# Optimization experiments

Hardware: AMD Instinct MI355X
Metric: run time of the kernel (lower is better)

## Reference

```python
import jax, jax.numpy as jnp
import numpy as np


def _mlp(h, weights, biases, n_relu):
    # Linear(+ReLU) stack; ReLU on the first n_relu layers, final layer linear only.
    for i, (w, b) in enumerate(zip(weights, biases)):
        h = h @ w + b
        if i < n_relu:
            h = jax.nn.relu(h)
    return h


def setup_inputs() -> dict:
    key = jax.random.key(0)
    ks = jax.random.split(key, 12)
    B, M, E = 16384, 512, 1024

    def lin(k, fan_in, fan_out):
        # xavier-ish scaling so activations stay well-conditioned
        return jax.random.normal(k, (fan_in, fan_out), jnp.float32) * (1.0 / np.sqrt(fan_in))

    return {
        "x": jax.random.normal(ks[0], (B, M), jnp.float32),
        "rand_noise": jax.random.uniform(ks[1], (B, M), jnp.float32),
        "u_random": jax.random.uniform(ks[2], (B, M), jnp.float32),
        "marginals_min": jnp.zeros((M,), jnp.float32),
        "marginals_max": jnp.ones((M,), jnp.float32),
        "enc_w0": lin(ks[3], M, E), "enc_b0": jnp.full((E,), 0.01, jnp.float32),
        "enc_w1": lin(ks[4], E, E), "enc_b1": jnp.full((E,), 0.01, jnp.float32),
        "enc_w2": lin(ks[5], E, E), "enc_b2": jnp.full((E,), 0.01, jnp.float32),
        "enc_w3": lin(ks[6], E, E), "enc_b3": jnp.full((E,), 0.01, jnp.float32),
        "head_w0": lin(ks[7], E, E), "head_b0": jnp.full((E,), 0.01, jnp.float32),
        "head_w1": lin(ks[8], E, E), "head_b1": jnp.full((E,), 0.01, jnp.float32),
        "corruption_len": 307,
    }


def reference(x, rand_noise, u_random, marginals_min, marginals_max,
              enc_w0, enc_b0, enc_w1, enc_b1, enc_w2, enc_b2, enc_w3, enc_b3,
              head_w0, head_b0, head_w1, head_b1, corruption_len):
    B, M = x.shape
    # Vectorized equivalent of per-row randperm(m)[:corruption_len]:
    # top-k of iid uniform noise picks a uniform random subset of size k per row.
    _, idx = jax.lax.top_k(rand_noise, corruption_len)            # [B, k]
    mask = jnp.zeros((B, M), bool).at[jnp.arange(B)[:, None], idx].set(True)

    # Marginal samples ~ Uniform(min, max) per feature.
    x_random = marginals_min + u_random * (marginals_max - marginals_min)
    x_corrupted = jnp.where(mask, x_random, x)

    enc_ws = [enc_w0, enc_w1, enc_w2, enc_w3]
    enc_bs = [enc_b0, enc_b1, enc_b2, enc_b3]
    head_ws = [head_w0, head_w1]
    head_bs = [head_b0, head_b1]

    # Run both branches through one batched pass (same math, fewer launches).
    both = jnp.concatenate([x, x_corrupted], axis=0)              # [2B, M]
    h = _mlp(both, enc_ws, enc_bs, n_relu=3)                      # encoder depth 4
    h = _mlp(h, head_ws, head_bs, n_relu=1)                       # head depth 2
    embeddings, embeddings_corrupted = h[:B], h[B:]
    return embeddings, embeddings_corrupted
```

## Files before the change

### kernel.cpp

```cpp
#include <hip/hip_runtime.h>

typedef _Float16 f16x8 __attribute__((ext_vector_type(8)));
typedef float f32x4 __attribute__((ext_vector_type(4)));

__device__ __forceinline__ void gload16(const void* g, void* l) {
  __builtin_amdgcn_global_load_lds(
      (const __attribute__((address_space(1))) void*)g,
      (__attribute__((address_space(3))) void*)l, 16, 0, 0);
}

__device__ __forceinline__ void barfence() {
  asm volatile("" ::: "memory");
  __builtin_amdgcn_s_barrier();
  asm volatile("" ::: "memory");
}

__device__ __forceinline__ int xcd_swz(int orig, int nwg) {
  int q = nwg >> 3, r = nwg & 7;
  int x = orig & 7, loc = orig >> 3;
  int base = (x < r) ? x * (q + 1) : r * (q + 1) + (x - r) * q;
  return base + loc;
}

struct WPtrs { const float* w[6]; _Float16* wt[6]; };
__global__ __launch_bounds__(256) void transpose_all(WPtrs p) {
  const int N = 1024;
  __shared__ float tile[32][33];
  int y = blockIdx.y, layer, ky;
  if (y < 16) { layer = 0; ky = y; }
  else { int t = y - 16; layer = 1 + (t >> 5); ky = t & 31; }
  int K = (layer == 0) ? 512 : 1024;
  const float* W = p.w[layer];
  _Float16* WT = p.wt[layer];
  int tx = threadIdx.x, ty = threadIdx.y;
  int n0 = blockIdx.x * 32, k0 = ky * 32;
#pragma unroll
  for (int i = 0; i < 4; i++)
    tile[ty + i * 8][tx] = W[(long)(k0 + ty + i * 8) * N + (n0 + tx)];
  __syncthreads();
#pragma unroll
  for (int i = 0; i < 4; i++)
    WT[(long)(n0 + ty + i * 8) * K + (k0 + tx)] = (_Float16)tile[tx][ty + i * 8];
}

__global__ __launch_bounds__(256) void cast_f16(const float* __restrict__ in,
                                                _Float16* __restrict__ out, long n) {
  long i = ((long)blockIdx.x * 256 + threadIdx.x) * 4;
  if (i < n) {
    float4 v = *(const float4*)(in + i);
    typedef _Float16 f16x4 __attribute__((ext_vector_type(4)));
    f16x4 o = {(_Float16)v.x, (_Float16)v.y, (_Float16)v.z, (_Float16)v.w};
    *(f16x4*)(out + i) = o;
  }
}

__global__ __launch_bounds__(256) void topk_corrupt(
    const float* __restrict__ noise, const float* __restrict__ x,
    const float* __restrict__ u, const float* __restrict__ mmin,
    const float* __restrict__ mmax, const int* __restrict__ kptr,
    _Float16* __restrict__ dplain, _Float16* __restrict__ dcorr,
    int xrow0, int nrows) {
  int lane = threadIdx.x & 63;
  int r = (blockIdx.x << 2) + (threadIdx.x >> 6);
  if (r >= nrows) return;
  long row = (long)xrow0 + r;
  long rb = row * 512 + lane * 8;
  float4 n0 = *(const float4*)(noise + rb);
  float4 n1 = *(const float4*)(noise + rb + 4);
  unsigned v[8] = {__float_as_uint(n0.x), __float_as_uint(n0.y),
                   __float_as_uint(n0.z), __float_as_uint(n0.w),
                   __float_as_uint(n1.x), __float_as_uint(n1.y),
                   __float_as_uint(n1.z), __float_as_uint(n1.w)};
  int kk = *kptr;
  unsigned T = 0;
  for (int bit = 30; bit >= 0; --bit) {
    unsigned Tp = T | (1u << bit);
    int c = 0;
#pragma unroll
    for (int j = 0; j < 8; j++) c += (int)__popcll(__ballot(v[j] >= Tp));
    if (c >= kk) T = Tp;
  }
  int cgt = 0;
  unsigned long long eqb[8];
#pragma unroll
  for (int j = 0; j < 8; j++) {
    cgt += (int)__popcll(__ballot(v[j] > T));
    eqb[j] = __ballot(v[j] == T);
  }
  int need = kk - cgt;
  unsigned long long below = (1ull << lane) - 1ull;
  int rank_base = 0;
#pragma unroll
  for (int j = 0; j < 8; j++) rank_base += (int)__popcll(eqb[j] & below);

  float4 x0 = *(const float4*)(x + rb);
  float4 x1 = *(const float4*)(x + rb + 4);
  float4 u0 = *(const float4*)(u + rb);
  float4 u1 = *(const float4*)(u + rb + 4);
  int col = lane * 8;
  float4 mn0 = *(const float4*)(mmin + col);
  float4 mn1 = *(const float4*)(mmin + col + 4);
  float4 mx0 = *(const float4*)(mmax + col);
  float4 mx1 = *(const float4*)(mmax + col + 4);
  float xs[8] = {x0.x, x0.y, x0.z, x0.w, x1.x, x1.y, x1.z, x1.w};
  float us[8] = {u0.x, u0.y, u0.z, u0.w, u1.x, u1.y, u1.z, u1.w};
  float mns[8] = {mn0.x, mn0.y, mn0.z, mn0.w, mn1.x, mn1.y, mn1.z, mn1.w};
  float mxs[8] = {mx0.x, mx0.y, mx0.z, mx0.w, mx1.x, mx1.y, mx1.z, mx1.w};

  f16x8 po, co;
  int loc = 0;
#pragma unroll
  for (int j = 0; j < 8; j++) {
    bool eq = (v[j] == T);
    int rank = rank_base + loc;
    bool m = (v[j] > T) || (eq && (rank < need));
    loc += eq ? 1 : 0;
    float rv = mns[j] + us[j] * (mxs[j] - mns[j]);
    float cv = m ? rv : xs[j];
    po[j] = (_Float16)xs[j];
    co[j] = (_Float16)cv;
  }
  long ob = (long)r * 512 + lane * 8;
  if (dplain) *(f16x8*)(dplain + ob) = po;
  *(f16x8*)(dcorr + ob) = co;
}

template <bool RELU, bool OUTF32>
__global__ __launch_bounds__(512, 2) void gemm8p(const _Float16* __restrict__ A,
                                                 const _Float16* __restrict__ BT,
                                                 const float* __restrict__ bias,
                                                 void* __restrict__ Cout, int K) {
  const int N = 1024;
  __shared__ _Float16 S[2][4][8192];
  int tid = threadIdx.x;
  int lane = tid & 63, wave = tid >> 6;
  int wr = wave >> 2, wc = wave & 3;
  int logical = xcd_swz(blockIdx.x, gridDim.x);
  long arow0 = (long)(logical >> 2) * 256;
  int bcol0 = (logical & 3) * 256;

  int srow = tid >> 3;
  int scg = (tid & 7) ^ (srow & 7);
  const _Float16* gA[2][2];
  const _Float16* gB[2][2];
#pragma unroll
  for (int h = 0; h < 2; h++)
#pragma unroll
    for (int j = 0; j < 2; j++) {
      gA[h][j] = A + (arow0 + h * 128 + j * 64 + srow) * (long)K + scg * 8;
      gB[h][j] = BT + (long)(bcol0 + h * 128 + j * 64 + srow) * K + scg * 8;
    }
  int lo = tid * 8;

#define STG_A(BUF, H, T)                                   \
  do {                                                     \
    gload16(gA[H][0] + (T) * 64, &S[BUF][H][lo]);          \
    gload16(gA[H][1] + (T) * 64, &S[BUF][H][4096 + lo]);   \
  } while (0)
#define STG_B(BUF, H, T)                                      \
  do {                                                        \
    gload16(gB[H][0] + (T) * 64, &S[BUF][2 + H][lo]);         \
    gload16(gB[H][1] + (T) * 64, &S[BUF][2 + H][4096 + lo]);  \
  } while (0)

  int lr = lane & 15, g = lane >> 4, e = lr & 7;
  int cs0 = ((0 * 4 + g) ^ e) * 8;
  int cs1 = ((1 * 4 + g) ^ e) * 8;
  int aoff[4], boff[2];
#pragma unroll
  for (int mf = 0; mf < 4; mf++) aoff[mf] = (wr * 64 + mf * 16 + lr) * 64;
#pragma unroll
  for (int nf = 0; nf < 2; nf++) boff[nf] = (wc * 32 + nf * 16 + lr) * 64;

  f16x8 af0[4][2], af1[4][2];
  f16x8 bf0[2][2], bf1[2][2];
  f32x4 acc[2][2][4][2] = {};

#define LDA(DST, BUF, MQ)                                            \
  do {                                                               \
    _Pragma("unroll") for (int mf = 0; mf < 4; mf++) {               \
      DST[mf][0] = *(const f16x8*)&S[BUF][MQ][aoff[mf] + cs0];       \
      DST[mf][1] = *(const f16x8*)&S[BUF][MQ][aoff[mf] + cs1];       \
    }                                                                \
  } while (0)
#define LDB(DST, BUF, NQ)                                            \
  do {                                                               \
    _Pragma("unroll") for (int nf = 0; nf < 2; nf++) {               \
      DST[nf][0] = *(const f16x8*)&S[BUF][2 + NQ][boff[nf] + cs0];   \
      DST[nf][1] = *(const f16x8*)&S[BUF][2 + NQ][boff[nf] + cs1];   \
    }                                                                \
  } while (0)
#define MFMA_Q(AF, BF, MQ, NQ)                                       \
  do {                                                               \
    __builtin_amdgcn_s_setprio(1);                                   \
    _Pragma("unroll") for (int mf = 0; mf < 4; mf++)                 \
    _Pragma("unroll") for (int nf = 0; nf < 2; nf++)                 \
    _Pragma("unroll") for (int kk = 0; kk < 2; kk++)                 \
      acc[MQ][NQ][mf][nf] = __builtin_amdgcn_mfma_f32_16x16x32_f16(  \
          AF[mf][kk], BF[nf][kk], acc[MQ][NQ][mf][nf], 0, 0, 0);     \
    __builtin_amdgcn_s_setprio(0);                                   \
  } while (0)

  int NT = K / 64;
  STG_B(0, 0, 0); STG_B(0, 1, 0); STG_A(0, 0, 0); STG_A(0, 1, 0);
  asm volatile("s_waitcnt vmcnt(2)" ::: "memory");
  barfence();
  LDA(af0, 0, 0);
  LDB(bf1, 0, 1);

  for (int t = 0; t < NT; ++t) {
    int buf = t & 1, nbuf = buf ^ 1;
    LDB(bf0, buf, 0);
    if (t + 1 < NT) { STG_B(nbuf, 0, t + 1); STG_B(nbuf, 1, t + 1); }
    MFMA_Q(af0, bf0, 0, 0);
    if (t + 1 < NT) asm volatile("s_waitcnt vmcnt(4)" ::: "memory");
    else            asm volatile("s_waitcnt vmcnt(0)" ::: "memory");
    barfence();
    LDA(af1, buf, 1);
    if (t + 1 < NT) STG_A(nbuf, 0, t + 1);
    MFMA_Q(af0, bf1, 0, 1);
    barfence();
    if (t + 1 < NT) STG_A(nbuf, 1, t + 1);
    MFMA_Q(af1, bf1, 1, 1);
    if (t + 1 < NT) asm volatile("s_waitcnt vmcnt(2)" ::: "memory");
    barfence();
    if (t + 1 < NT) { LDA(af0, nbuf, 0); LDB(bf1, nbuf, 1); }
    MFMA_Q(af1, bf0, 1, 0);
    if (t + 1 < NT) barfence();
  }
#undef STG_A
#undef STG_B
#undef LDA
#undef LDB
#undef MFMA_Q

  int r0 = (lane >> 4) * 4;
  float bv[2][2];
#pragma unroll
  for (int nq = 0; nq < 2; nq++)
#pragma unroll
    for (int nf = 0; nf < 2; nf++)
      bv[nq][nf] = bias[bcol0 + nq * 128 + wc * 32 + nf * 16 + lr];
#pragma unroll
  for (int mq = 0; mq < 2; mq++)
#pragma unroll
    for (int mf = 0; mf < 4; mf++) {
      long rowb = arow0 + mq * 128 + wr * 64 + mf * 16 + r0;
#pragma unroll
      for (int nq = 0; nq < 2; nq++)
#pragma unroll
        for (int nf = 0; nf < 2; nf++) {
          int col = bcol0 + nq * 128 + wc * 32 + nf * 16 + lr;
#pragma unroll
          for (int rr = 0; rr < 4; rr++) {
            float v = acc[mq][nq][mf][nf][rr] + bv[nq][nf];
            if (RELU) v = fmaxf(v, 0.f);
            if (OUTF32) ((float*)Cout)[(rowb + rr) * N + col] = v;
            else ((_Float16*)Cout)[(rowb + rr) * N + col] = (_Float16)v;
          }
        }
    }
}

extern "C" void kernel_launch(void* const* d_in, const int* in_sizes, int n_in,
                              void* d_out, int out_size, void* d_ws, size_t ws_size,
                              hipStream_t stream) {
  const float* x    = (const float*)d_in[0];
  const float* rn   = (const float*)d_in[1];
  const float* ur   = (const float*)d_in[2];
  const float* mmin = (const float*)d_in[3];
  const float* mmax = (const float*)d_in[4];
  const float* W[6]  = {(const float*)d_in[5],  (const float*)d_in[7],  (const float*)d_in[9],
                        (const float*)d_in[11], (const float*)d_in[13], (const float*)d_in[15]};
  const float* Bi[6] = {(const float*)d_in[6],  (const float*)d_in[8],  (const float*)d_in[10],
                        (const float*)d_in[12], (const float*)d_in[14], (const float*)d_in[16]};
  const int* kptr = (const int*)d_in[17];
  float* out = (float*)d_out;

  const long B = 16384;
  const int E = 1024;
  const int Ks[6] = {512, 1024, 1024, 1024, 1024, 1024};

  char* ws = (char*)d_ws;
  _Float16* wT[6];
  size_t off = 0;
  for (int i = 0; i < 6; i++) { wT[i] = (_Float16*)(ws + off); off += (size_t)Ks[i] * E * 2; }
  size_t rem = (ws_size > off) ? ws_size - off : 0;
  long R = 32768;
  while (R > 256 && (size_t)R * 5120 > rem) R >>= 1;

  _Float16* bothc = (_Float16*)(ws + off);
  _Float16* h0 = bothc + R * 512;
  _Float16* h1 = h0 + R * 1024;

  WPtrs wp;
  for (int i = 0; i < 6; i++) { wp.w[i] = W[i]; wp.wt[i] = wT[i]; }
  transpose_all<<<dim3(E / 32, 16 + 5 * 32), dim3(32, 8), 0, stream>>>(wp);

  for (long r0 = 0; r0 < 2 * B; r0 += R) {
    if (R == 2 * B) {
      topk_corrupt<<<dim3((unsigned)(B / 4)), dim3(256), 0, stream>>>(
          rn, x, ur, mmin, mmax, kptr, bothc, bothc + B * 512, 0, (int)B);
    } else {
      long plainEnd = (r0 < B) ? ((r0 + R < B) ? (r0 + R) : B) : r0;
      long p1 = plainEnd - r0;
      if (p1 > 0) {
        long n = p1 * 512;
        long blocks = (n / 4 + 255) / 256;
        cast_f16<<<dim3((unsigned)blocks), dim3(256), 0, stream>>>(x + r0 * 512, bothc, n);
      }
      long c0 = (r0 > B) ? r0 : B;
      long p2 = (r0 + R) - c0;
      if (p2 > 0) {
        topk_corrupt<<<dim3((unsigned)((p2 + 3) / 4)), dim3(256), 0, stream>>>(
            rn, x, ur, mmin, mmax, kptr, (_Float16*)nullptr,
            bothc + (c0 - r0) * 512, (int)(c0 - B), (int)p2);
      }
    }
    dim3 gg((unsigned)((R / 256) * 4)), gb(512);
    gemm8p<true,  false><<<gg, gb, 0, stream>>>(bothc, wT[0], Bi[0], (void*)h0, 512);
    gemm8p<true,  false><<<gg, gb, 0, stream>>>(h0,    wT[1], Bi[1], (void*)h1, 1024);
    gemm8p<true,  false><<<gg, gb, 0, stream>>>(h1,    wT[2], Bi[2], (void*)h0, 1024);
    gemm8p<false, false><<<gg, gb, 0, stream>>>(h0,    wT[3], Bi[3], (void*)h1, 1024);
    gemm8p<true,  false><<<gg, gb, 0, stream>>>(h1,    wT[4], Bi[4], (void*)h0, 1024);
    gemm8p<false, true ><<<gg, gb, 0, stream>>>(h0,    wT[5], Bi[5],
                                                 (void*)(out + r0 * 1024), 1024);
  }
}
```

Before: 404.7 us.

## Shrink GEMM tiles to 128x128, fuse transpose with top-k prep, nontemporal output

Cuts the GEMM block tile from 256x256 to 128x128 with half the LDS and a launch bound allowing 4 blocks per CU. This raises the block count and occupancy at the cost of less data reuse per block. The weight transpose and the top-k/corruption prep are merged into one launch, and the final fp32 output is written with nontemporal stores. The waitcnt values are retuned for fewer loads per stage.

```diff
diff --git a/kernel.cpp b/kernel.cpp
--- a/kernel.cpp
+++ b/kernel.cpp
@@ -23,47 +23,13 @@
 }
 
 struct WPtrs { const float* w[6]; _Float16* wt[6]; };
-__global__ __launch_bounds__(256) void transpose_all(WPtrs p) {
-  const int N = 1024;
-  __shared__ float tile[32][33];
-  int y = blockIdx.y, layer, ky;
-  if (y < 16) { layer = 0; ky = y; }
-  else { int t = y - 16; layer = 1 + (t >> 5); ky = t & 31; }
-  int K = (layer == 0) ? 512 : 1024;
-  const float* W = p.w[layer];
-  _Float16* WT = p.wt[layer];
-  int tx = threadIdx.x, ty = threadIdx.y;
-  int n0 = blockIdx.x * 32, k0 = ky * 32;
-#pragma unroll
-  for (int i = 0; i < 4; i++)
-    tile[ty + i * 8][tx] = W[(long)(k0 + ty + i * 8) * N + (n0 + tx)];
-  __syncthreads();
-#pragma unroll
-  for (int i = 0; i < 4; i++)
-    WT[(long)(n0 + ty + i * 8) * K + (k0 + tx)] = (_Float16)tile[tx][ty + i * 8];
-}
-
-__global__ __launch_bounds__(256) void cast_f16(const float* __restrict__ in,
-                                                _Float16* __restrict__ out, long n) {
-  long i = ((long)blockIdx.x * 256 + threadIdx.x) * 4;
-  if (i < n) {
-    float4 v = *(const float4*)(in + i);
-    typedef _Float16 f16x4 __attribute__((ext_vector_type(4)));
-    f16x4 o = {(_Float16)v.x, (_Float16)v.y, (_Float16)v.z, (_Float16)v.w};
-    *(f16x4*)(out + i) = o;
-  }
-}
-
-__global__ __launch_bounds__(256) void topk_corrupt(
+
+__device__ __forceinline__ void topk_row(
     const float* __restrict__ noise, const float* __restrict__ x,
     const float* __restrict__ u, const float* __restrict__ mmin,
-    const float* __restrict__ mmax, const int* __restrict__ kptr,
-    _Float16* __restrict__ dplain, _Float16* __restrict__ dcorr,
-    int xrow0, int nrows) {
+    const float* __restrict__ mmax, int kk, _Float16* __restrict__ dplain,
+    _Float16* __restrict__ dcorr, long row, long orow) {
   int lane = threadIdx.x & 63;
-  int r = (blockIdx.x << 2) + (threadIdx.x >> 6);
-  if (r >= nrows) return;
-  long row = (long)xrow0 + r;
   long rb = row * 512 + lane * 8;
   float4 n0 = *(const float4*)(noise + rb);
   float4 n1 = *(const float4*)(noise + rb + 4);
@@ -71,7 +37,6 @@
                    __float_as_uint(n0.z), __float_as_uint(n0.w),
                    __float_as_uint(n1.x), __float_as_uint(n1.y),
                    __float_as_uint(n1.z), __float_as_uint(n1.w)};
-  int kk = *kptr;
   unsigned T = 0;
   for (int bit = 30; bit >= 0; --bit) {
     unsigned Tp = T | (1u << bit);
@@ -120,90 +85,151 @@
     po[j] = (_Float16)xs[j];
     co[j] = (_Float16)cv;
   }
-  long ob = (long)r * 512 + lane * 8;
+  long ob = orow * 512 + lane * 8;
   if (dplain) *(f16x8*)(dplain + ob) = po;
   *(f16x8*)(dcorr + ob) = co;
 }
 
+__global__ __launch_bounds__(256) void prep_all(
+    const float* __restrict__ noise, const float* __restrict__ x,
+    const float* __restrict__ u, const float* __restrict__ mmin,
+    const float* __restrict__ mmax, const int* __restrict__ kptr,
+    _Float16* __restrict__ dplain, _Float16* __restrict__ dcorr,
+    WPtrs p, int ntopk) {
+  const int N = 1024;
+  if ((int)blockIdx.x < ntopk) {
+    int r = ((int)blockIdx.x << 2) + (threadIdx.x >> 6);
+    topk_row(noise, x, u, mmin, mmax, *kptr, dplain, dcorr, r, r);
+    return;
+  }
+  int b = (int)blockIdx.x - ntopk;
+  int bx = b & 31;
+  int y = b >> 5;
+  __shared__ float tile[32][33];
+  int layer, ky;
+  if (y < 16) { layer = 0; ky = y; }
+  else { int t = y - 16; layer = 1 + (t >> 5); ky = t & 31; }
+  int K = (layer == 0) ? 512 : 1024;
+  const float* W = p.w[layer];
+  _Float16* WT = p.wt[layer];
+  int tx = threadIdx.x & 31, ty = threadIdx.x >> 5;
+  int n0 = bx * 32, k0 = ky * 32;
+#pragma unroll
+  for (int i = 0; i < 4; i++)
+    tile[ty + i * 8][tx] = W[(long)(k0 + ty + i * 8) * N + (n0 + tx)];
+  __syncthreads();
+#pragma unroll
+  for (int i = 0; i < 4; i++)
+    WT[(long)(n0 + ty + i * 8) * K + (k0 + tx)] = (_Float16)tile[tx][ty + i * 8];
+}
+
+__global__ __launch_bounds__(256) void transpose_all(WPtrs p) {
+  const int N = 1024;
+  __shared__ float tile[32][33];
+  int y = blockIdx.y, layer, ky;
+  if (y < 16) { layer = 0; ky = y; }
+  else { int t = y - 16; layer = 1 + (t >> 5); ky = t & 31; }
+  int K = (layer == 0) ? 512 : 1024;
+  const float* W = p.w[layer];
+  _Float16* WT = p.wt[layer];
+  int tx = threadIdx.x, ty = threadIdx.y;
+  int n0 = blockIdx.x * 32, k0 = ky * 32;
+#pragma unroll
+  for (int i = 0; i < 4; i++)
+    tile[ty + i * 8][tx] = W[(long)(k0 + ty + i * 8) * N + (n0 + tx)];
+  __syncthreads();
+#pragma unroll
+  for (int i = 0; i < 4; i++)
+    WT[(long)(n0 + ty + i * 8) * K + (k0 + tx)] = (_Float16)tile[tx][ty + i * 8];
+}
+
+__global__ __launch_bounds__(256) void cast_f16(const float* __restrict__ in,
+                                                _Float16* __restrict__ out, long n) {
+  long i = ((long)blockIdx.x * 256 + threadIdx.x) * 4;
+  if (i < n) {
+    float4 v = *(const float4*)(in + i);
+    typedef _Float16 f16x4 __attribute__((ext_vector_type(4)));
+    f16x4 o = {(_Float16)v.x, (_Float16)v.y, (_Float16)v.z, (_Float16)v.w};
+    *(f16x4*)(out + i) = o;
+  }
+}
+
+__global__ __launch_bounds__(256) void topk_corrupt(
+    const float* __restrict__ noise, const float* __restrict__ x,
+    const float* __restrict__ u, const float* __restrict__ mmin,
+    const float* __restrict__ mmax, const int* __restrict__ kptr,
+    _Float16* __restrict__ dcorr, int xrow0, int nrows) {
+  int r = ((int)blockIdx.x << 2) + (threadIdx.x >> 6);
+  if (r >= nrows) return;
+  topk_row(noise, x, u, mmin, mmax, *kptr, (_Float16*)nullptr, dcorr,
+           (long)xrow0 + r, r);
+}
+
 template <bool RELU, bool OUTF32>
-__global__ __launch_bounds__(512, 2) void gemm8p(const _Float16* __restrict__ A,
+__global__ __launch_bounds__(512, 4) void gemmtp(const _Float16* __restrict__ A,
                                                  const _Float16* __restrict__ BT,
                                                  const float* __restrict__ bias,
                                                  void* __restrict__ Cout, int K) {
   const int N = 1024;
-  __shared__ _Float16 S[2][4][8192];
+  __shared__ _Float16 S[2][4][4096];
   int tid = threadIdx.x;
   int lane = tid & 63, wave = tid >> 6;
   int wr = wave >> 2, wc = wave & 3;
   int logical = xcd_swz(blockIdx.x, gridDim.x);
-  long arow0 = (long)(logical >> 2) * 256;
-  int bcol0 = (logical & 3) * 256;
+  long arow0 = (long)(logical >> 3) * 128;
+  int bcol0 = (logical & 7) * 128;
 
   int srow = tid >> 3;
   int scg = (tid & 7) ^ (srow & 7);
-  const _Float16* gA[2][2];
-  const _Float16* gB[2][2];
-#pragma unroll
-  for (int h = 0; h < 2; h++)
-#pragma unroll
-    for (int j = 0; j < 2; j++) {
-      gA[h][j] = A + (arow0 + h * 128 + j * 64 + srow) * (long)K + scg * 8;
-      gB[h][j] = BT + (long)(bcol0 + h * 128 + j * 64 + srow) * K + scg * 8;
-    }
+  const _Float16* gA[2];
+  const _Float16* gB[2];
+#pragma unroll
+  for (int h = 0; h < 2; h++) {
+    gA[h] = A + (arow0 + h * 64 + srow) * (long)K + scg * 8;
+    gB[h] = BT + (long)(bcol0 + h * 64 + srow) * K + scg * 8;
+  }
   int lo = tid * 8;
 
-#define STG_A(BUF, H, T)                                   \
-  do {                                                     \
-    gload16(gA[H][0] + (T) * 64, &S[BUF][H][lo]);          \
-    gload16(gA[H][1] + (T) * 64, &S[BUF][H][4096 + lo]);   \
-  } while (0)
-#define STG_B(BUF, H, T)                                      \
-  do {                                                        \
-    gload16(gB[H][0] + (T) * 64, &S[BUF][2 + H][lo]);         \
-    gload16(gB[H][1] + (T) * 64, &S[BUF][2 + H][4096 + lo]);  \
-  } while (0)
+#define STG_A(BUF, H, T) gload16(gA[H] + (T) * 64, &S[BUF][H][lo])
+#define STG_B(BUF, H, T) gload16(gB[H] + (T) * 64, &S[BUF][2 + H][lo])
 
   int lr = lane & 15, g = lane >> 4, e = lr & 7;
   int cs0 = ((0 * 4 + g) ^ e) * 8;
   int cs1 = ((1 * 4 + g) ^ e) * 8;
-  int aoff[4], boff[2];
-#pragma unroll
-  for (int mf = 0; mf < 4; mf++) aoff[mf] = (wr * 64 + mf * 16 + lr) * 64;
-#pragma unroll
-  for (int nf = 0; nf < 2; nf++) boff[nf] = (wc * 32 + nf * 16 + lr) * 64;
-
-  f16x8 af0[4][2], af1[4][2];
-  f16x8 bf0[2][2], bf1[2][2];
-  f32x4 acc[2][2][4][2] = {};
+  int aoff[2];
+#pragma unroll
+  for (int mf = 0; mf < 2; mf++) aoff[mf] = (wr * 32 + mf * 16 + lr) * 64;
+  int boff = (wc * 16 + lr) * 64;
+
+  f16x8 af0[2][2], af1[2][2];
+  f16x8 bf0[2], bf1[2];
+  f32x4 acc[2][2][2] = {};
 
 #define LDA(DST, BUF, MQ)                                            \
   do {                                                               \
-    _Pragma("unroll") for (int mf = 0; mf < 4; mf++) {               \
+    _Pragma("unroll") for (int mf = 0; mf < 2; mf++) {               \
       DST[mf][0] = *(const f16x8*)&S[BUF][MQ][aoff[mf] + cs0];       \
       DST[mf][1] = *(const f16x8*)&S[BUF][MQ][aoff[mf] + cs1];       \
     }                                                                \
   } while (0)
 #define LDB(DST, BUF, NQ)                                            \
   do {                                                               \
-    _Pragma("unroll") for (int nf = 0; nf < 2; nf++) {               \
-      DST[nf][0] = *(const f16x8*)&S[BUF][2 + NQ][boff[nf] + cs0];   \
-      DST[nf][1] = *(const f16x8*)&S[BUF][2 + NQ][boff[nf] + cs1];   \
-    }                                                                \
+    DST[0] = *(const f16x8*)&S[BUF][2 + NQ][boff + cs0];             \
+    DST[1] = *(const f16x8*)&S[BUF][2 + NQ][boff + cs1];             \
   } while (0)
 #define MFMA_Q(AF, BF, MQ, NQ)                                       \
   do {                                                               \
     __builtin_amdgcn_s_setprio(1);                                   \
-    _Pragma("unroll") for (int mf = 0; mf < 4; mf++)                 \
-    _Pragma("unroll") for (int nf = 0; nf < 2; nf++)                 \
+    _Pragma("unroll") for (int mf = 0; mf < 2; mf++)                 \
     _Pragma("unroll") for (int kk = 0; kk < 2; kk++)                 \
-      acc[MQ][NQ][mf][nf] = __builtin_amdgcn_mfma_f32_16x16x32_f16(  \
-          AF[mf][kk], BF[nf][kk], acc[MQ][NQ][mf][nf], 0, 0, 0);     \
+      acc[MQ][NQ][mf] = __builtin_amdgcn_mfma_f32_16x16x32_f16(      \
+          AF[mf][kk], BF[kk], acc[MQ][NQ][mf], 0, 0, 0);             \
     __builtin_amdgcn_s_setprio(0);                                   \
   } while (0)
 
   int NT = K / 64;
   STG_B(0, 0, 0); STG_B(0, 1, 0); STG_A(0, 0, 0); STG_A(0, 1, 0);
-  asm volatile("s_waitcnt vmcnt(2)" ::: "memory");
+  asm volatile("s_waitcnt vmcnt(1)" ::: "memory");
   barfence();
   LDA(af0, 0, 0);
   LDB(bf1, 0, 1);
@@ -213,7 +239,7 @@
     LDB(bf0, buf, 0);
     if (t + 1 < NT) { STG_B(nbuf, 0, t + 1); STG_B(nbuf, 1, t + 1); }
     MFMA_Q(af0, bf0, 0, 0);
-    if (t + 1 < NT) asm volatile("s_waitcnt vmcnt(4)" ::: "memory");
+    if (t + 1 < NT) asm volatile("s_waitcnt vmcnt(2)" ::: "memory");
     else            asm volatile("s_waitcnt vmcnt(0)" ::: "memory");
     barfence();
     LDA(af1, buf, 1);
@@ -222,7 +248,7 @@
     barfence();
     if (t + 1 < NT) STG_A(nbuf, 1, t + 1);
     MFMA_Q(af1, bf1, 1, 1);
-    if (t + 1 < NT) asm volatile("s_waitcnt vmcnt(2)" ::: "memory");
+    if (t + 1 < NT) asm volatile("s_waitcnt vmcnt(1)" ::: "memory");
     barfence();
     if (t + 1 < NT) { LDA(af0, nbuf, 0); LDB(bf1, nbuf, 1); }
     MFMA_Q(af1, bf0, 1, 0);
@@ -235,30 +261,28 @@
 #undef MFMA_Q
 
   int r0 = (lane >> 4) * 4;
-  float bv[2][2];
-#pragma unroll
-  for (int nq = 0; nq < 2; nq++)
-#pragma unroll
-    for (int nf = 0; nf < 2; nf++)
-      bv[nq][nf] = bias[bcol0 + nq * 128 + wc * 32 + nf * 16 + lr];
+  float bv[2];
+#pragma unroll
+  for (int nq = 0; nq < 2; nq++) bv[nq] = bias[bcol0 + nq * 64 + wc * 16 + lr];
 #pragma unroll
   for (int mq = 0; mq < 2; mq++)
 #pragma unroll
-    for (int mf = 0; mf < 4; mf++) {
-      long rowb = arow0 + mq * 128 + wr * 64 + mf * 16 + r0;
-#pragma unroll
-      for (int nq = 0; nq < 2; nq++)
-#pragma unroll
-        for (int nf = 0; nf < 2; nf++) {
-          int col = bcol0 + nq * 128 + wc * 32 + nf * 16 + lr;
-#pragma unroll
-          for (int rr = 0; rr < 4; rr++) {
-            float v = acc[mq][nq][mf][nf][rr] + bv[nq][nf];
-            if (RELU) v = fmaxf(v, 0.f);
-            if (OUTF32) ((float*)Cout)[(rowb + rr) * N + col] = v;
-            else ((_Float16*)Cout)[(rowb + rr) * N + col] = (_Float16)v;
+    for (int mf = 0; mf < 2; mf++) {
+      long rowb = arow0 + mq * 64 + wr * 32 + mf * 16 + r0;
+#pragma unroll
+      for (int nq = 0; nq < 2; nq++) {
+        int col = bcol0 + nq * 64 + wc * 16 + lr;
+#pragma unroll
+        for (int rr = 0; rr < 4; rr++) {
+          float v = acc[mq][nq][mf][rr] + bv[nq];
+          if (RELU) v = fmaxf(v, 0.f);
+          if (OUTF32) {
+            __builtin_nontemporal_store(v, &((float*)Cout)[(rowb + rr) * N + col]);
+          } else {
+            ((_Float16*)Cout)[(rowb + rr) * N + col] = (_Float16)v;
           }
         }
+      }
     }
 }
 
@@ -295,13 +319,22 @@
 
   WPtrs wp;
   for (int i = 0; i < 6; i++) { wp.w[i] = W[i]; wp.wt[i] = wT[i]; }
-  transpose_all<<<dim3(E / 32, 16 + 5 * 32), dim3(32, 8), 0, stream>>>(wp);
-
-  for (long r0 = 0; r0 < 2 * B; r0 += R) {
-    if (R == 2 * B) {
-      topk_corrupt<<<dim3((unsigned)(B / 4)), dim3(256), 0, stream>>>(
-          rn, x, ur, mmin, mmax, kptr, bothc, bothc + B * 512, 0, (int)B);
-    } else {
+
+  if (R == 2 * B) {
+    int ntopk = (int)(B / 4);
+    prep_all<<<dim3((unsigned)(ntopk + 32 * 176)), dim3(256), 0, stream>>>(
+        rn, x, ur, mmin, mmax, kptr, bothc, bothc + B * 512, wp, ntopk);
+
+    dim3 gg((unsigned)((R / 128) * 8)), gb(512);
+    gemmtp<true,  false><<<gg, gb, 0, stream>>>(bothc, wT[0], Bi[0], (void*)h0, 512);
+    gemmtp<true,  false><<<gg, gb, 0, stream>>>(h0,    wT[1], Bi[1], (void*)h1, 1024);
+    gemmtp<true,  false><<<gg, gb, 0, stream>>>(h1,    wT[2], Bi[2], (void*)h0, 1024);
+    gemmtp<false, false><<<gg, gb, 0, stream>>>(h0,    wT[3], Bi[3], (void*)h1, 1024);
+    gemmtp<true,  false><<<gg, gb, 0, stream>>>(h1,    wT[4], Bi[4], (void*)h0, 1024);
+    gemmtp<false, true ><<<gg, gb, 0, stream>>>(h0,    wT[5], Bi[5], (void*)out, 1024);
+  } else {
+    transpose_all<<<dim3(E / 32, 16 + 5 * 32), dim3(32, 8), 0, stream>>>(wp);
+    for (long r0 = 0; r0 < 2 * B; r0 += R) {
       long plainEnd = (r0 < B) ? ((r0 + R < B) ? (r0 + R) : B) : r0;
       long p1 = plainEnd - r0;
       if (p1 > 0) {
@@ -313,17 +346,17 @@
       long p2 = (r0 + R) - c0;
       if (p2 > 0) {
         topk_corrupt<<<dim3((unsigned)((p2 + 3) / 4)), dim3(256), 0, stream>>>(
-            rn, x, ur, mmin, mmax, kptr, (_Float16*)nullptr,
-            bothc + (c0 - r0) * 512, (int)(c0 - B), (int)p2);
+            rn, x, ur, mmin, mmax, kptr, bothc + (c0 - r0) * 512,
+            (int)(c0 - B), (int)p2);
       }
+      dim3 gg((unsigned)((R / 128) * 8)), gb(512);
+      gemmtp<true,  false><<<gg, gb, 0, stream>>>(bothc, wT[0], Bi[0], (void*)h0, 512);
+      gemmtp<true,  false><<<gg, gb, 0, stream>>>(h0,    wT[1], Bi[1], (void*)h1, 1024);
+      gemmtp<true,  false><<<gg, gb, 0, stream>>>(h1,    wT[2], Bi[2], (void*)h0, 1024);
+      gemmtp<false, false><<<gg, gb, 0, stream>>>(h0,    wT[3], Bi[3], (void*)h1, 1024);
+      gemmtp<true,  false><<<gg, gb, 0, stream>>>(h1,    wT[4], Bi[4], (void*)h0, 1024);
+      gemmtp<false, true ><<<gg, gb, 0, stream>>>(h0,    wT[5], Bi[5],
+                                                  (void*)(out + r0 * 1024), 1024);
     }
-    dim3 gg((unsigned)((R / 256) * 4)), gb(512);
-    gemm8p<true,  false><<<gg, gb, 0, stream>>>(bothc, wT[0], Bi[0], (void*)h0, 512);
-    gemm8p<true,  false><<<gg, gb, 0, stream>>>(h0,    wT[1], Bi[1], (void*)h1, 1024);
-    gemm8p<true,  false><<<gg, gb, 0, stream>>>(h1,    wT[2], Bi[2], (void*)h0, 1024);
-    gemm8p<false, false><<<gg, gb, 0, stream>>>(h0,    wT[3], Bi[3], (void*)h1, 1024);
-    gemm8p<true,  false><<<gg, gb, 0, stream>>>(h1,    wT[4], Bi[4], (void*)h0, 1024);
-    gemm8p<false, true ><<<gg, gb, 0, stream>>>(h0,    wT[5], Bi[5],
-                                                 (void*)(out + r0 * 1024), 1024);
-  }
-}
+  }
+}
```

Measured after the change: 460.3 us. 1.14x slower.
